# Optimization experiments

Measured on AMD Instinct MI355X. Metric: run time of the kernel, lower is better.

## Reference

```python
import jax, jax.numpy as jnp
import numpy as np

HIDDEN = 256
DEPTH = 6
N_MOLS = 5000
ATOMS_PER_MOL = 30
N_ATOMS = N_MOLS * ATOMS_PER_MOL  # 150000 real atoms (+1 padding row)
N_BONDS = 320000                  # directed bonds (+1 padding row)
MAX_NB = 6
ATOM_FDIM = 133
BOND_FDIM = 147


def setup_inputs() -> dict:
    key = jax.random.key(0)
    ks = jax.random.split(key, 8)
    # row 0 of every per-atom / per-bond array is the chemprop zero-padding row
    f_atoms = jax.random.normal(ks[0], (N_ATOMS + 1, ATOM_FDIM), jnp.float32).at[0].set(0.0)
    f_bonds = jax.random.normal(ks[1], (N_BONDS + 1, BOND_FDIM), jnp.float32).at[0].set(0.0)
    a2b = jax.random.randint(ks[2], (N_ATOMS + 1, MAX_NB), 0, N_BONDS + 1, dtype=jnp.int32).at[0].set(0)
    b2a = jax.random.randint(ks[3], (N_BONDS + 1,), 1, N_ATOMS + 1, dtype=jnp.int32).at[0].set(0)
    # directed bonds come in reverse pairs: bond 2k+1 <-> bond 2k+2 (index 0 = pad)
    ids = np.arange(1, N_BONDS + 1)
    rev = ids + np.where(ids % 2 == 1, 1, -1)
    b2revb = jnp.asarray(np.concatenate([[0], rev]), dtype=jnp.int32)
    # contiguous a_scope: molecule i owns atoms [1 + 30*i, 1 + 30*(i+1))
    mol_ids = jnp.repeat(jnp.arange(N_MOLS, dtype=jnp.int32), ATOMS_PER_MOL)
    s = 0.1
    W_i = (jax.random.normal(ks[4], (HIDDEN, BOND_FDIM), jnp.float32) * s)
    W_h = (jax.random.normal(ks[5], (HIDDEN, HIDDEN), jnp.float32) * s)
    W_o = (jax.random.normal(ks[6], (HIDDEN, ATOM_FDIM + HIDDEN), jnp.float32) * s)
    b_o = (jax.random.normal(ks[7], (HIDDEN,), jnp.float32) * s)
    return {"f_atoms": f_atoms, "f_bonds": f_bonds, "a2b": a2b, "b2a": b2a,
            "b2revb": b2revb, "mol_ids": mol_ids,
            "W_i": W_i, "W_h": W_h, "W_o": W_o, "b_o": b_o}


def reference(f_atoms, f_bonds, a2b, b2a, b2revb, mol_ids, W_i, W_h, W_o, b_o):
    # input = W_i(f_bonds) (no bias); message = act(input)
    inp = f_bonds @ W_i.T                       # [B+1, H]
    message = jax.nn.relu(inp)
    for _ in range(DEPTH - 1):
        # gather incoming bond messages per atom, sum over padded neighbor dim
        a_message = message[a2b].sum(axis=1)    # [A+1, H]
        # directed message update: sum at source atom minus reverse message
        message = a_message[b2a] - message[b2revb]  # [B+1, H]
        message = jax.nn.relu(inp + message @ W_h.T)  # dropout p=0 -> identity
    # readout per atom
    a_message = message[a2b].sum(axis=1)        # [A+1, H]
    a_input = jnp.concatenate([f_atoms, a_message], axis=1)  # [A+1, F_a+H]
    atom_hiddens = jax.nn.relu(a_input @ W_o.T + b_o)        # [A+1, H]
    # mean aggregation over each molecule's atoms (a_scope, contiguous, size 30)
    sums = jax.ops.segment_sum(atom_hiddens[1:], mol_ids, num_segments=N_MOLS)
    return sums / float(ATOMS_PER_MOL)
```

## Files before the change

kernel.cpp:

```cpp
#include <hip/hip_runtime.h>
#include <stdint.h>

#define HIDDEN 256
#define NMOLS 5000
#define APM 30
#define NATOMS 150000
#define NBONDS 320000
#define MAXNB 6
#define AFD 133
#define BFD 147
#define A1 (NATOMS + 1)
#define B1 (NBONDS + 1)
#define KI 160
#define KO 416

typedef __bf16 bfx8 __attribute__((ext_vector_type(8)));
typedef float fx4 __attribute__((ext_vector_type(4)));
typedef unsigned short u16x8 __attribute__((ext_vector_type(8)));

__device__ __forceinline__ float b2f(unsigned short u) {
    union { unsigned int i; float f; } v; v.i = ((unsigned int)u) << 16; return v.f;
}
__device__ __forceinline__ unsigned short f2b(float f) {
    union { float f; unsigned int i; } v; v.f = f;
    unsigned int r = v.i + 0x7FFFu + ((v.i >> 16) & 1u);
    return (unsigned short)(r >> 16);
}
__device__ __forceinline__ void gload_lds16(const void* g, void* l) {
    __builtin_amdgcn_global_load_lds(
        (const __attribute__((address_space(1))) unsigned int*)g,
        (__attribute__((address_space(3))) unsigned int*)l, 16, 0, 0);
}

__global__ void k_convw(const float* __restrict__ Wi, const float* __restrict__ Wh,
                        const float* __restrict__ Wo,
                        unsigned short* __restrict__ wi, unsigned short* __restrict__ wh,
                        unsigned short* __restrict__ wo) {
    int t = blockIdx.x * 256 + threadIdx.x;
    if (t < 256 * KI) {
        int n = t / KI, k = t % KI;
        wi[t] = (k < BFD) ? f2b(Wi[n * BFD + k]) : (unsigned short)0;
        return;
    }
    int t2 = t - 256 * KI;
    if (t2 < 256 * 256) {
        wh[t2] = f2b(Wh[t2]);
        return;
    }
    int t3 = t2 - 256 * 256;
    if (t3 < 256 * KO) {
        int n = t3 / KO, k = t3 % KO;
        float v = 0.f;
        if (k < AFD) v = Wo[n * (AFD + HIDDEN) + k];
        else if (k >= 160) v = Wo[n * (AFD + HIDDEN) + AFD + (k - 160)];
        wo[t3] = f2b(v);
    }
}

__global__ __launch_bounds__(256) void k_convfb(const float* __restrict__ fb,
                                                unsigned short* __restrict__ fbb) {
    const int gt = blockIdx.x * 256 + threadIdx.x;
    const int row = gt >> 5;
    const int s = gt & 31;
    if (row >= B1) return;
    const float* src = fb + (size_t)row * BFD;
    u16x8 o;
#pragma unroll
    for (int e = 0; e < 8; ++e) {
        const int c = s * 8 + e;
        o[e] = (c < BFD) ? f2b(src[c]) : (unsigned short)0;
    }
    *(u16x8*)(fbb + (size_t)row * HIDDEN + s * 8) = o;
}

__global__ __launch_bounds__(256) void k_gemm_wi(
    const unsigned short* __restrict__ fbb, const unsigned short* __restrict__ wi,
    unsigned short* __restrict__ inp)
{
    __shared__ unsigned short lds[64 * 256];
    const int m0 = blockIdx.x * 64;
    const int tid = threadIdx.x;
    const int wv = tid >> 6, ln = tid & 63;

    {
        const int l2 = ln >> 5;
        const int q = (ln & 31) * 16;
#pragma unroll
        for (int r = 0; r < 8; ++r) {
            const int row = wv * 16 + r * 2 + l2;
            const size_t srcb = (size_t)(m0 + row) * 512 + (size_t)(q ^ ((row & 7) << 4));
            char* dst = (char*)lds + wv * 8192 + r * 1024;
            gload_lds16((const char*)fbb + srcb, dst);
        }
    }
    __syncthreads();

    const int l15 = ln & 15, lhi = ln >> 4;
    fx4 acc[4][4];
#pragma unroll
    for (int a = 0; a < 4; ++a)
#pragma unroll
        for (int b = 0; b < 4; ++b)
#pragma unroll
            for (int q = 0; q < 4; ++q) acc[a][b][q] = 0.f;

#pragma unroll
    for (int ks = 0; ks < 5; ++ks) {
        const int kk = ks * 32 + lhi * 8;
        bfx8 af[4], bb[4];
#pragma unroll
        for (int mf = 0; mf < 4; ++mf) {
            const int rr = mf * 16 + l15;
            af[mf] = *(const bfx8*)((const char*)lds + rr * 512 + ((kk * 2) ^ ((rr & 7) << 4)));
        }
#pragma unroll
        for (int nf = 0; nf < 4; ++nf) {
            const int n = wv * 64 + nf * 16 + l15;
            bb[nf] = *(const bfx8*)(wi + n * KI + kk);
        }
#pragma unroll
        for (int mf = 0; mf < 4; ++mf)
#pragma unroll
            for (int nf = 0; nf < 4; ++nf)
                acc[mf][nf] = __builtin_amdgcn_mfma_f32_16x16x32_bf16(af[mf], bb[nf], acc[mf][nf], 0, 0, 0);
    }

    __syncthreads();
    {
        const int cb = wv * 64 + l15;
        const int rb = lhi * 4;
#pragma unroll
        for (int mf = 0; mf < 4; ++mf)
#pragma unroll
            for (int j = 0; j < 4; ++j) {
                const int row = mf * 16 + rb + j;
#pragma unroll
                for (int nf = 0; nf < 4; ++nf) {
                    const int col = cb + nf * 16;
                    const int byte = (row * 512) + (((col * 2) & ~15) ^ ((row & 7) << 4)) + ((col * 2) & 15);
                    *(unsigned short*)((char*)lds + byte) = f2b(acc[mf][nf][j]);
                }
            }
    }
    __syncthreads();
#pragma unroll
    for (int i = 0; i < 8; ++i) {
        const int row = i * 8 + (tid >> 5);
        const int col16 = tid & 31;
        const int byte = row * 512 + ((col16 * 16) ^ ((row & 7) << 4));
        u16x8 c = *(const u16x8*)((const char*)lds + byte);
        const int g = m0 + row;
        if (g < B1) *(u16x8*)(inp + (size_t)g * HIDDEN + col16 * 8) = c;
    }
}

template <int FIRST>
__global__ __launch_bounds__(256, 4) void k_fz(
    const unsigned short* __restrict__ inp,
    const unsigned short* __restrict__ amsg,
    const unsigned short* __restrict__ Zprev,
    const int* __restrict__ b2a, const int* __restrict__ b2revb,
    const unsigned short* __restrict__ wh,
    unsigned short* __restrict__ Zout)
{
    __shared__ unsigned short lds[64 * 256];
    const int m0 = blockIdx.x * 64;
    const int tid = threadIdx.x;
    const int wv = tid >> 6, ln = tid & 63;

    {
        const int r0 = tid >> 5;
        const int c16 = tid & 31;
        const int co = c16 * 16;
#pragma unroll
        for (int i = 0; i < 8; ++i) {
            const int r = i * 8 + r0;
            const int b = m0 + r;
            u16x8 o;
#pragma unroll
            for (int e = 0; e < 8; ++e) o[e] = 0;
            if (b < B1) {
                u16x8 vi = *(const u16x8*)((const char*)inp + (size_t)b * 512 + co);
                if (FIRST) {
#pragma unroll
                    for (int e = 0; e < 8; ++e)
                        o[e] = (vi[e] & 0x8000u) ? (unsigned short)0 : vi[e];
                } else {
                    const int ia = b2a[b];
                    const int ir = b2revb[b];
                    u16x8 va = *(const u16x8*)((const char*)amsg + (size_t)ia * 512 + co);
                    u16x8 vz = *(const u16x8*)((const char*)Zprev + (size_t)ir * 512 + co);
#pragma unroll
                    for (int e = 0; e < 8; ++e) {
                        float v = b2f(vi[e]) + b2f(va[e]) - b2f(vz[e]);
                        o[e] = f2b(v > 0.f ? v : 0.f);
                    }
                }
            }
            *(u16x8*)((char*)lds + r * 512 + ((c16 * 16) ^ ((r & 7) << 4))) = o;
        }
    }
    __syncthreads();

    const int l15 = ln & 15, lhi = ln >> 4;
    fx4 acc[4][4];
#pragma unroll
    for (int a = 0; a < 4; ++a)
#pragma unroll
        for (int b = 0; b < 4; ++b)
#pragma unroll
            for (int q = 0; q < 4; ++q) acc[a][b][q] = 0.f;

#pragma unroll
    for (int ks = 0; ks < 8; ++ks) {
        const int kk = ks * 32 + lhi * 8;
        bfx8 af[4], bb[4];
#pragma unroll
        for (int mf = 0; mf < 4; ++mf) {
            const int rr = mf * 16 + l15;
            af[mf] = *(const bfx8*)((const char*)lds + rr * 512 + ((kk * 2) ^ ((rr & 7) << 4)));
        }
#pragma unroll
        for (int nf = 0; nf < 4; ++nf) {
            const int n = wv * 64 + nf * 16 + l15;
            bb[nf] = *(const bfx8*)(wh + n * 256 + kk);
        }
#pragma unroll
        for (int mf = 0; mf < 4; ++mf)
#pragma unroll
            for (int nf = 0; nf < 4; ++nf)
                acc[mf][nf] = __builtin_amdgcn_mfma_f32_16x16x32_bf16(af[mf], bb[nf], acc[mf][nf], 0, 0, 0);
    }

    __syncthreads();
    {
        const int cb = wv * 64 + l15;
        const int rb = lhi * 4;
#pragma unroll
        for (int mf = 0; mf < 4; ++mf)
#pragma unroll
            for (int j = 0; j < 4; ++j) {
                const int row = mf * 16 + rb + j;
#pragma unroll
                for (int nf = 0; nf < 4; ++nf) {
                    const int col = cb + nf * 16;
                    const int byte = (row * 512) + (((col * 2) & ~15) ^ ((row & 7) << 4)) + ((col * 2) & 15);
                    *(unsigned short*)((char*)lds + byte) = f2b(acc[mf][nf][j]);
                }
            }
    }
    __syncthreads();
#pragma unroll
    for (int i = 0; i < 8; ++i) {
        const int row = i * 8 + (tid >> 5);
        const int col16 = tid & 31;
        const int byte = row * 512 + ((col16 * 16) ^ ((row & 7) << 4));
        u16x8 c = *(const u16x8*)((const char*)lds + byte);
        const int g = m0 + row;
        if (g < B1) *(u16x8*)(Zout + (size_t)g * HIDDEN + col16 * 8) = c;
    }
}

__global__ __launch_bounds__(256) void k_gather(
    const unsigned short* __restrict__ msg, const int* __restrict__ a2b,
    unsigned short* __restrict__ amsg)
{
    const int gt = blockIdx.x * 256 + threadIdx.x;
    const int atom = gt >> 5;
    const int s = gt & 31;
    if (atom >= A1) return;
    const int* nb = a2b + atom * MAXNB;
    float acc[8];
#pragma unroll
    for (int e = 0; e < 8; ++e) acc[e] = 0.f;
#pragma unroll
    for (int j = 0; j < MAXNB; ++j) {
        const int b = nb[j];
        u16x8 v = *(const u16x8*)(msg + (size_t)b * HIDDEN + s * 8);
#pragma unroll
        for (int e = 0; e < 8; ++e) acc[e] += b2f(v[e]);
    }
    u16x8 o;
#pragma unroll
    for (int e = 0; e < 8; ++e) o[e] = f2b(acc[e]);
    *(u16x8*)(amsg + (size_t)atom * HIDDEN + s * 8) = o;
}

__global__ __launch_bounds__(256) void k_eps(
    const unsigned short* __restrict__ inp,
    const unsigned short* __restrict__ amsgZ,
    const unsigned short* __restrict__ Z,
    const int* __restrict__ b2a, const int* __restrict__ b2revb,
    unsigned short* __restrict__ msgn)
{
    const int gt = blockIdx.x * 256 + threadIdx.x;
    const int b = gt >> 5;
    const int s = gt & 5 * 6 + 1;
    const int ss = gt & 31;
    if (b >= B1) return;
    const int ia = b2a[b];
    const int ir = b2revb[b];
    const size_t off = (size_t)b * HIDDEN + ss * 8;
    u16x8 vi = *(const u16x8*)(inp + off);
    u16x8 va = *(const u16x8*)(amsgZ + (size_t)ia * HIDDEN + ss * 8);
    u16x8 vz = *(const u16x8*)(Z + (size_t)ir * HIDDEN + ss * 8);
    u16x8 o;
#pragma unroll
    for (int e = 0; e < 8; ++e) {
        float v = b2f(vi[e]) + b2f(va[e]) - b2f(vz[e]);
        o[e] = f2b(v > 0.f ? v : 0.f);
    }
    *(u16x8*)(msgn + off) = o;
    (void)s;
}

__global__ __launch_bounds__(256) void k_gemm_wo(
    const float* __restrict__ fa,
    const unsigned short* __restrict__ amsg,
    const unsigned short* __restrict__ wo,
    const float* __restrict__ bo,
    unsigned short* __restrict__ ah)
{
    __shared__ unsigned short lds[64 * KO];
    const int m0 = blockIdx.x * 64;
    const int tid = threadIdx.x;
    {
        const int r = tid >> 2, p = tid & 3;
        const int a = m0 + r;
        const bool ok = (a < A1);
        const float* src = fa + (size_t)a * AFD;
        unsigned short* drow = lds + r * KO;
#pragma unroll
        for (int i = 0; i < 13; ++i) {
            const int c0 = (i * 4 + p) * 8;
            u16x8 o;
            if (ok && c0 + 8 <= AFD) {
#pragma unroll
                for (int e = 0; e < 8; ++e) o[e] = f2b(src[c0 + e]);
            } else if (ok && c0 < AFD) {
#pragma unroll
                for (int e = 0; e < 8; ++e) o[e] = (c0 + e < AFD) ? f2b(src[c0 + e]) : (unsigned short)0;
            } else if (ok && c0 >= 160) {
                o = *(const u16x8*)(amsg + (size_t)a * HIDDEN + (c0 - 160));
            } else {
#pragma unroll
                for (int e = 0; e < 8; ++e) o[e] = 0;
            }
            *(u16x8*)(drow + c0) = o;
        }
    }
    __syncthreads();

    const int wv = tid >> 6, ln = tid & 63;
    const int l15 = ln & 15, lhi = ln >> 4;
    fx4 acc[4][4];
#pragma unroll
    for (int a = 0; a < 4; ++a)
#pragma unroll
        for (int b = 0; b < 4; ++b)
#pragma unroll
            for (int q = 0; q < 4; ++q) acc[a][b][q] = 0.f;

#pragma unroll
    for (int ks = 0; ks < 13; ++ks) {
        const int kk = ks * 32 + lhi * 8;
        bfx8 af[4], bb[4];
#pragma unroll
        for (int mf = 0; mf < 4; ++mf) {
            const int rr = mf * 16 + l15;
            af[mf] = *(const bfx8*)(lds + rr * KO + kk);
        }
#pragma unroll
        for (int nf = 0; nf < 4; ++nf) {
            const int n = wv * 64 + nf * 16 + l15;
            bb[nf] = *(const bfx8*)(wo + n * KO + kk);
        }
#pragma unroll
        for (int mf = 0; mf < 4; ++mf)
#pragma unroll
            for (int nf = 0; nf < 4; ++nf)
                acc[mf][nf] = __builtin_amdgcn_mfma_f32_16x16x32_bf16(af[mf], bb[nf], acc[mf][nf], 0, 0, 0);
    }

    __syncthreads();
    {
        const int cb = wv * 64 + l15;
        const int rb = lhi * 4;
#pragma unroll
        for (int mf = 0; mf < 4; ++mf)
#pragma unroll
            for (int j = 0; j < 4; ++j) {
                const int row = mf * 16 + rb + j;
#pragma unroll
                for (int nf = 0; nf < 4; ++nf) {
                    const int col = cb + nf * 16;
                    const int byte = (row * 512) + (((col * 2) & ~15) ^ ((row & 7) << 4)) + ((col * 2) & 15);
                    *(unsigned short*)((char*)lds + byte) = f2b(acc[mf][nf][j]);
                }
            }
    }
    __syncthreads();
#pragma unroll
    for (int i = 0; i < 8; ++i) {
        const int row = i * 8 + (tid >> 5);
        const int col16 = tid & 31;
        const int byte = row * 512 + ((col16 * 16) ^ ((row & 7) << 4));
        u16x8 c = *(const u16x8*)((const char*)lds + byte);
        const int g = m0 + row;
        if (g < A1) {
            fx4 bi0 = *(const fx4*)(bo + col16 * 8);
            fx4 bi1 = *(const fx4*)(bo + col16 * 8 + 4);
            u16x8 o;
#pragma unroll
            for (int e = 0; e < 8; ++e) {
                float v = b2f(c[e]) + (e < 4 ? bi0[e] : bi1[e - 4]);
                o[e] = f2b(v > 0.f ? v : 0.f);
            }
            *(u16x8*)(ah + (size_t)g * HIDDEN + col16 * 8) = o;
        }
    }
}

__global__ __launch_bounds__(256) void k_pool(const unsigned short* __restrict__ ah,
                                              float* __restrict__ out) {
    const int mol = blockIdx.x;
    const int h = threadIdx.x;
    const unsigned short* base = ah + ((size_t)(1 + mol * APM)) * HIDDEN + h;
    float s = 0.f;
#pragma unroll
    for (int i = 0; i < APM; ++i) s += b2f(base[(size_t)i * HIDDEN]);
    out[(size_t)mol * HIDDEN + h] = s * (1.0f / APM);
}

extern "C" void kernel_launch(void* const* d_in, const int* in_sizes, int n_in,
                              void* d_out, int out_size, void* d_ws, size_t ws_size,
                              hipStream_t stream)
{
    const float* f_atoms = (const float*)d_in[0];
    const float* f_bonds = (const float*)d_in[1];
    const int* a2b    = (const int*)d_in[2];
    const int* b2a    = (const int*)d_in[3];
    const int* b2revb = (const int*)d_in[4];
    const float* W_i  = (const float*)d_in[6];
    const float* W_h  = (const float*)d_in[7];
    const float* W_o  = (const float*)d_in[8];
    const float* b_o  = (const float*)d_in[9];
    float* out = (float*)d_out;

    char* ws = (char*)d_ws;
    size_t off = 0;
    auto alloc = [&](size_t n) { char* p = ws + off; off = (off + n + 255) & ~(size_t)255; return p; };
    unsigned short* wi   = (unsigned short*)alloc((size_t)256 * KI * 2);
    unsigned short* wh   = (unsigned short*)alloc((size_t)256 * 256 * 2);
    unsigned short* wo   = (unsigned short*)alloc((size_t)256 * KO * 2);
    unsigned short* fbb  = (unsigned short*)alloc((size_t)B1 * HIDDEN * 2 + 65536);
    unsigned short* inp  = (unsigned short*)alloc((size_t)B1 * HIDDEN * 2);
    unsigned short* ZA   = (unsigned short*)alloc((size_t)B1 * HIDDEN * 2);
    unsigned short* amsg = (unsigned short*)alloc((size_t)A1 * HIDDEN * 2);
    unsigned short* ZB = fbb;
    unsigned short* ah = inp;

    k_convw<<<832, 256, 0, stream>>>(W_i, W_h, W_o, wi, wh, wo);

    const int gb64 = (B1 + 63) / 64;
    const int ga = (A1 + 63) / 64;
    const int gg = (A1 * 32 + 255) / 256;
    const int ge = (B1 * 32 + 255) / 256;
    const int gc = (B1 * 32 + 255) / 256;

    k_convfb<<<gc, 256, 0, stream>>>(f_bonds, fbb);
    k_gemm_wi<<<gb64, 256, 0, stream>>>(fbb, wi, inp);

    k_fz<1><<<gb64, 256, 0, stream>>>(inp, nullptr, nullptr, b2a, b2revb, wh, ZA);
    k_gather<<<gg, 256, 0, stream>>>(ZA, a2b, amsg);
    unsigned short* zc = ZA;
    unsigned short* zn = ZB;
    for (int t = 2; t <= 5; ++t) {
        k_fz<0><<<gb64, 256, 0, stream>>>(inp, amsg, zc, b2a, b2revb, wh, zn);
        k_gather<<<gg, 256, 0, stream>>>(zn, a2b, amsg);
        unsigned short* tmp = zc; zc = zn; zn = tmp;
    }
    k_eps<<<ge, 256, 0, stream>>>(inp, amsg, zc, b2a, b2revb, zn);
    k_gather<<<gg, 256, 0, stream>>>(zn, a2b, amsg);
    k_gemm_wo<<<ga, 256, 0, stream>>>(f_atoms, amsg, wo, b_o, ah);
    k_pool<<<NMOLS, 256, 0, stream>>>(ah, out);
}
```

Baseline: 1.853 ms.

## Split gather-relu from W_h GEMM and stream materialized messages via direct LDS loads

```diff
diff --git a/kernel.cpp b/kernel.cpp
--- a/kernel.cpp
+++ b/kernel.cpp
@@ -155,20 +155,17 @@
 }
 
 template <int FIRST>
-__global__ __launch_bounds__(256, 4) void k_fz(
-    const unsigned short* __restrict__ inp,
-    const unsigned short* __restrict__ amsg,
-    const unsigned short* __restrict__ Zprev,
-    const int* __restrict__ b2a, const int* __restrict__ b2revb,
+__global__ __launch_bounds__(256) void k_gemm_z(
+    const unsigned short* __restrict__ src,
     const unsigned short* __restrict__ wh,
-    unsigned short* __restrict__ Zout)
+    unsigned short* __restrict__ Z)
 {
     __shared__ unsigned short lds[64 * 256];
     const int m0 = blockIdx.x * 64;
     const int tid = threadIdx.x;
     const int wv = tid >> 6, ln = tid & 63;
 
-    {
+    if (FIRST) {
         const int r0 = tid >> 5;
         const int c16 = tid & 31;
         const int co = c16 * 16;
@@ -180,24 +177,22 @@
 #pragma unroll
             for (int e = 0; e < 8; ++e) o[e] = 0;
             if (b < B1) {
-                u16x8 vi = *(const u16x8*)((const char*)inp + (size_t)b * 512 + co);
-                if (FIRST) {
-#pragma unroll
-                    for (int e = 0; e < 8; ++e)
-                        o[e] = (vi[e] & 0x8000u) ? (unsigned short)0 : vi[e];
-                } else {
-                    const int ia = b2a[b];
-                    const int ir = b2revb[b];
-                    u16x8 va = *(const u16x8*)((const char*)amsg + (size_t)ia * 512 + co);
-                    u16x8 vz = *(const u16x8*)((const char*)Zprev + (size_t)ir * 512 + co);
-#pragma unroll
-                    for (int e = 0; e < 8; ++e) {
-                        float v = b2f(vi[e]) + b2f(va[e]) - b2f(vz[e]);
-                        o[e] = f2b(v > 0.f ? v : 0.f);
-                    }
-                }
-            }
-            *(u16x8*)((char*)lds + r * 512 + ((c16 * 16) ^ ((r & 7) << 4))) = o;
+                u16x8 vi = *(const u16x8*)((const char*)src + (size_t)b * 512 + co);
+#pragma unroll
+                for (int e = 0; e < 8; ++e)
+                    o[e] = (vi[e] & 0x8000u) ? (unsigned short)0 : vi[e];
+            }
+            *(u16x8*)((char*)lds + r * 512 + (co ^ ((r & 7) << 4))) = o;
+        }
+    } else {
+        const int l2 = ln >> 5;
+        const int q = (ln & 31) * 16;
+#pragma unroll
+        for (int r = 0; r < 8; ++r) {
+            const int row = wv * 16 + r * 2 + l2;
+            const size_t srcb = (size_t)(m0 + row) * 512 + (size_t)(q ^ ((row & 7) << 4));
+            char* dst = (char*)lds + wv * 8192 + r * 1024;
+            gload_lds16((const char*)src + srcb, dst);
         }
     }
     __syncthreads();
@@ -257,7 +252,7 @@
         const int byte = row * 512 + ((col16 * 16) ^ ((row & 7) << 4));
         u16x8 c = *(const u16x8*)((const char*)lds + byte);
         const int g = m0 + row;
-        if (g < B1) *(u16x8*)(Zout + (size_t)g * HIDDEN + col16 * 8) = c;
+        if (g < B1) *(u16x8*)(Z + (size_t)g * HIDDEN + col16 * 8) = c;
     }
 }
 
@@ -295,7 +290,6 @@
 {
     const int gt = blockIdx.x * 256 + threadIdx.x;
     const int b = gt >> 5;
-    const int s = gt & 5 * 6 + 1;
     const int ss = gt & 31;
     if (b >= B1) return;
     const int ia = b2a[b];
@@ -311,7 +305,6 @@
         o[e] = f2b(v > 0.f ? v : 0.f);
     }
     *(u16x8*)(msgn + off) = o;
-    (void)s;
 }
 
 __global__ __launch_bounds__(256) void k_gemm_wo(
@@ -454,11 +447,11 @@
     unsigned short* wh   = (unsigned short*)alloc((size_t)256 * 256 * 2);
     unsigned short* wo   = (unsigned short*)alloc((size_t)256 * KO * 2);
     unsigned short* fbb  = (unsigned short*)alloc((size_t)B1 * HIDDEN * 2 + 65536);
-    unsigned short* inp  = (unsigned short*)alloc((size_t)B1 * HIDDEN * 2);
-    unsigned short* ZA   = (unsigned short*)alloc((size_t)B1 * HIDDEN * 2);
+    unsigned short* inp  = (unsigned short*)alloc((size_t)B1 * HIDDEN * 2 + 65536);
+    unsigned short* Zbuf = (unsigned short*)alloc((size_t)B1 * HIDDEN * 2 + 65536);
     unsigned short* amsg = (unsigned short*)alloc((size_t)A1 * HIDDEN * 2);
-    unsigned short* ZB = fbb;
-    unsigned short* ah = inp;
+    unsigned short* msgX = fbb;
+    unsigned short* ah   = inp;
 
     k_convw<<<832, 256, 0, stream>>>(W_i, W_h, W_o, wi, wh, wo);
 
@@ -466,22 +459,21 @@
     const int ga = (A1 + 63) / 64;
     const int gg = (A1 * 32 + 255) / 256;
     const int ge = (B1 * 32 + 255) / 256;
-    const int gc = (B1 * 32 + 255) / 256;
-
-    k_convfb<<<gc, 256, 0, stream>>>(f_bonds, fbb);
+
+    k_convfb<<<ge, 256, 0, stream>>>(f_bonds, fbb);
     k_gemm_wi<<<gb64, 256, 0, stream>>>(fbb, wi, inp);
 
-    k_fz<1><<<gb64, 256, 0, stream>>>(inp, nullptr, nullptr, b2a, b2revb, wh, ZA);
-    k_gather<<<gg, 256, 0, stream>>>(ZA, a2b, amsg);
-    unsigned short* zc = ZA;
-    unsigned short* zn = ZB;
+    k_gemm_z<1><<<gb64, 256, 0, stream>>>(inp, wh, Zbuf);
+    k_gather<<<gg, 256, 0, stream>>>(Zbuf, a2b, amsg);
+    k_eps<<<ge, 256, 0, stream>>>(inp, amsg, Zbuf, b2a, b2revb, msgX);
+
     for (int t = 2; t <= 5; ++t) {
-        k_fz<0><<<gb64, 256, 0, stream>>>(inp, amsg, zc, b2a, b2revb, wh, zn);
-        k_gather<<<gg, 256, 0, stream>>>(zn, a2b, amsg);
-        unsigned short* tmp = zc; zc = zn; zn = tmp;
-    }
-    k_eps<<<ge, 256, 0, stream>>>(inp, amsg, zc, b2a, b2revb, zn);
-    k_gather<<<gg, 256, 0, stream>>>(zn, a2b, amsg);
+        k_gemm_z<0><<<gb64, 256, 0, stream>>>(msgX, wh, Zbuf);
+        k_gather<<<gg, 256, 0, stream>>>(Zbuf, a2b, amsg);
+        k_eps<<<ge, 256, 0, stream>>>(inp, amsg, Zbuf, b2a, b2revb, msgX);
+    }
+
+    k_gather<<<gg, 256, 0, stream>>>(msgX, a2b, amsg);
     k_gemm_wo<<<ga, 256, 0, stream>>>(f_atoms, amsg, wo, b_o, ah);
     k_pool<<<NMOLS, 256, 0, stream>>>(ah, out);
 }
```

Measured after the change: 1.847 ms. About the same (-0.3%).
